# Optimization experiments

Hardware: AMD Instinct MI355X
Metric: run time of the kernel (lower is better)

The kernel has to match this reference:

```python
import jax, jax.numpy as jnp
import numpy as np
from jax import lax

START_TAG = 29
STOP_TAG = 30
PAD_TAG = 31
NEG_INF = -10000.0


def setup_inputs() -> dict:
    key = jax.random.key(0)
    k_feat, k_trans, k_len = jax.random.split(key, 3)
    S, B, T = 1024, 1024, 32
    feats = jax.random.normal(k_feat, (S, B, T), dtype=jnp.float32)
    # left-aligned padding mask with random lengths in [S//2, S]
    lengths = jax.random.randint(k_len, (B,), S // 2, S + 1)
    mask = (jnp.arange(S)[:, None] < lengths[None, :]).astype(jnp.float32)  # [S,B]
    transitions = jax.random.normal(k_trans, (T, T), dtype=jnp.float32)
    # replicate the constraint initialization from __init__
    transitions = transitions.at[START_TAG, :].set(NEG_INF)
    transitions = transitions.at[:, STOP_TAG].set(NEG_INF)
    transitions = transitions.at[:, PAD_TAG].set(NEG_INF)
    transitions = transitions.at[PAD_TAG, :].set(NEG_INF)
    transitions = transitions.at[PAD_TAG, STOP_TAG].set(0.0)
    transitions = transitions.at[PAD_TAG, PAD_TAG].set(0.0)
    # zero emissions at padded steps, as _get_lstm_features does (feats * mask)
    feats = feats * mask[:, :, None]
    return {"feats": feats, "mask": mask, "transitions": transitions}


def reference(feats, mask, transitions):
    """CRF forward algorithm (log partition) + Viterbi max-score scan.

    feats: [S, B, T] emission scores, mask: [S, B] float, transitions: [T, T]
    (transitions[i, j] = score of transitioning from tag j to tag i).
    Returns (logZ [B], best_score [B], pointers [S, B, T] int32).
    """
    S, B, T = feats.shape

    alpha0 = jnp.full((B, T), NEG_INF, dtype=feats.dtype).at[:, START_TAG].set(0.0)

    def fwd_step(alpha, xs):
        feat, m = xs  # feat [B,T], m [B]
        # alpha_t[b, i, j] = alpha[b, j] + transitions[i, j] + feat[b, i]
        alpha_t = alpha[:, None, :] + transitions[None, :, :] + feat[:, :, None]
        new = jax.nn.logsumexp(alpha_t, axis=-1)  # [B,T]
        m = m[:, None]
        return new * m + alpha * (1.0 - m), None

    alpha, _ = lax.scan(fwd_step, alpha0, (feats, mask))
    logZ = jax.nn.logsumexp(alpha + transitions[STOP_TAG][None, :], axis=-1)  # [B]

    def vit_step(scores, xs):
        feat, m = xs
        scores_t = scores[:, None, :] + transitions[None, :, :]  # [B,T,T]
        best = jnp.max(scores_t, axis=-1)                        # [B,T]
        ptr = jnp.argmax(scores_t, axis=-1).astype(jnp.int32)    # [B,T]
        scores_t = best + feat
        m = m[:, None]
        return scores_t * m + scores * (1.0 - m), ptr

    scores0 = jnp.full((B, T), NEG_INF, dtype=feats.dtype).at[:, START_TAG].set(0.0)
    scores, pointers = lax.scan(vit_step, scores0, (feats, mask))
    scores = scores + transitions[STOP_TAG][None, :]
    best_score = jnp.max(scores, axis=-1)  # [B]
    return logZ, best_score, pointers
```

## Files before the change

### kernel.cpp

```cpp
#include <hip/hip_runtime.h>


#define SS 1024
#define BB 1024
#define TT 32
#define POFF (2 * BB)

static __device__ __forceinline__ float fastrcp(float x) {
#if __has_builtin(__builtin_amdgcn_rcpf)
  return __builtin_amdgcn_rcpf(x);
#else
  return 1.0f / x;
#endif
}

__global__ __launch_bounds__(64, 1) void crf3_kernel(
    const float* __restrict__ feats,
    const float* __restrict__ mask,
    const float* __restrict__ trans,
    float* __restrict__ out) {

  const int l  = threadIdx.x;
  const int h  = l >> 5;
  const int i  = l & 31;
  const int b0 = blockIdx.x * 2;
  const int b  = b0 + h;

  __shared__ __align__(16) float row[64];

  const float* fbase = feats + (size_t)b0 * TT + l;
  const float* mbase = mask + b;
  const float t_stop = trans[30 * TT + i];

  float fA[4], mA[4], fB[4], mB[4];
#pragma unroll
  for (int u = 0; u < 4; ++u) {
    fA[u] = fbase[(size_t)u * (BB * TT)];
    mA[u] = mbase[(size_t)u * BB];
    fB[u] = fbase[(size_t)(u + 4) * (BB * TT)];
    mB[u] = mbase[(size_t)(u + 4) * BB];
  }

  if (blockIdx.y == 0) {
    float er[32];
#pragma unroll
    for (int k = 0; k < 32; ++k)
      er[k] = __expf(trans[i * TT + k]);

    float p = (i == 29) ? 1.0f : 0.0f;
    float C = 0.0f;

    auto fstep = [&](float fv, float mv) {
      bool act = (mv != 0.0f);
      float ef = __expf(fv);
      row[l] = p;
      __builtin_amdgcn_wave_barrier();
      const float4* q = (const float4*)&row[h * 32];
      float4 q0 = q[0], q1 = q[1], q2 = q[2], q3 = q[3];
      float4 q4 = q[4], q5 = q[5], q6 = q[6], q7 = q[7];
      __builtin_amdgcn_wave_barrier();
      float q0c = fmaxf(q0.x, 1e-20f);
      float r = fastrcp(q0c);
      float a0 = er[0] * q0.x, a1 = er[1] * q0.y;
      float a2 = er[2] * q0.z, a3 = er[3] * q0.w;
      a0 = fmaf(er[4],  q1.x, a0); a1 = fmaf(er[5],  q1.y, a1);
      a2 = fmaf(er[6],  q1.z, a2); a3 = fmaf(er[7],  q1.w, a3);
      a0 = fmaf(er[8],  q2.x, a0); a1 = fmaf(er[9],  q2.y, a1);
      a2 = fmaf(er[10], q2.z, a2); a3 = fmaf(er[11], q2.w, a3);
      a0 = fmaf(er[12], q3.x, a0); a1 = fmaf(er[13], q3.y, a1);
      a2 = fmaf(er[14], q3.z, a2); a3 = fmaf(er[15], q3.w, a3);
      a0 = fmaf(er[16], q4.x, a0); a1 = fmaf(er[17], q4.y, a1);
      a2 = fmaf(er[18], q4.z, a2); a3 = fmaf(er[19], q4.w, a3);
      a0 = fmaf(er[20], q5.x, a0); a1 = fmaf(er[21], q5.y, a1);
      a2 = fmaf(er[22], q5.z, a2); a3 = fmaf(er[23], q5.w, a3);
      a0 = fmaf(er[24], q6.x, a0); a1 = fmaf(er[25], q6.y, a1);
      a2 = fmaf(er[26], q6.z, a2); a3 = fmaf(er[27], q6.w, a3);
      a0 = fmaf(er[28], q7.x, a0); a1 = fmaf(er[29], q7.y, a1);
      a2 = fmaf(er[30], q7.z, a2); a3 = fmaf(er[31], q7.w, a3);
      float D = (a0 + a1) + (a2 + a3);
      float pn = D * r * ef;
      p = act ? pn : p;
      C += act ? __logf(q0c) : 0.0f;
    };

#pragma unroll 1
    for (int s = 0; s < SS; s += 8) {
      if (__ballot(mA[0] != 0.0f) == 0ull) goto fwd_done;
#pragma unroll
      for (int u = 0; u < 4; ++u) fstep(fA[u], mA[u]);
#pragma unroll
      for (int u = 0; u < 4; ++u) {
        int su = s + 8 + u; su = (su < SS) ? su : 0;
        fA[u] = fbase[(size_t)su * (BB * TT)];
        mA[u] = mbase[(size_t)su * BB];
      }
      if (__ballot(mB[0] != 0.0f) == 0ull) goto fwd_done;
#pragma unroll
      for (int u = 0; u < 4; ++u) fstep(fB[u], mB[u]);
#pragma unroll
      for (int u = 0; u < 4; ++u) {
        int su = s + 12 + u; su = (su < SS) ? su : 0;
        fB[u] = fbase[(size_t)su * (BB * TT)];
        mB[u] = mbase[(size_t)su * BB];
      }
    }
fwd_done:
    {
      float alpha = C + __logf(p);
      float v = alpha + t_stop;
      float M2 = v;
#pragma unroll
      for (int d = 1; d < 32; d <<= 1) M2 = fmaxf(M2, __shfl_xor(M2, d, 64));
      float e = __expf(v - M2);
#pragma unroll
      for (int d = 1; d < 32; d <<= 1) e += __shfl_xor(e, d, 64);
      if (i == 0) out[b] = M2 + __logf(e);
    }
    return;
  }

  {
    float tr[32];
#pragma unroll
    for (int k = 0; k < 32; ++k) tr[k] = trans[i * TT + k];

    float sc = (i == 29) ? 0.0f : -10000.0f;
    int s_exit = SS;

    auto vstep = [&](float& best, int& ptr) {
      row[l] = sc;
      __builtin_amdgcn_wave_barrier();
      const float4* q = (const float4*)&row[h * 32];
      float4 q0 = q[0], q1 = q[1], q2 = q[2], q3 = q[3];
      float4 q4 = q[4], q5 = q[5], q6 = q[6], q7 = q[7];
      __builtin_amdgcn_wave_barrier();
      float v[32];
      v[0]  = q0.x + tr[0];  v[1]  = q0.y + tr[1];
      v[2]  = q0.z + tr[2];  v[3]  = q0.w + tr[3];
      v[4]  = q1.x + tr[4];  v[5]  = q1.y + tr[5];
      v[6]  = q1.z + tr[6];  v[7]  = q1.w + tr[7];
      v[8]  = q2.x + tr[8];  v[9]  = q2.y + tr[9];
      v[10] = q2.z + tr[10]; v[11] = q2.w + tr[11];
      v[12] = q3.x + tr[12]; v[13] = q3.y + tr[13];
      v[14] = q3.z + tr[14]; v[15] = q3.w + tr[15];
      v[16] = q4.x + tr[16]; v[17] = q4.y + tr[17];
      v[18] = q4.z + tr[18]; v[19] = q4.w + tr[19];
      v[20] = q5.x + tr[20]; v[21] = q5.y + tr[21];
      v[22] = q5.z + tr[22]; v[23] = q5.w + tr[23];
      v[24] = q6.x + tr[24]; v[25] = q6.y + tr[25];
      v[26] = q6.z + tr[26]; v[27] = q6.w + tr[27];
      v[28] = q7.x + tr[28]; v[29] = q7.y + tr[29];
      v[30] = q7.z + tr[30]; v[31] = q7.w + tr[31];
      int ix[32];
#pragma unroll
      for (int k = 0; k < 32; ++k) ix[k] = k;
#pragma unroll
      for (int st = 1; st < 32; st <<= 1) {
#pragma unroll
        for (int k = 0; k < 32; k += 2 * st) {
          bool t = v[k + st] > v[k];
          v[k]  = t ? v[k + st] : v[k];
          ix[k] = t ? ix[k + st] : ix[k];
        }
      }
      best = v[0];
      ptr  = ix[0];
    };

#pragma unroll 1
    for (int s = 0; s < SS; s += 8) {
      if (__ballot(mA[0] != 0.0f) == 0ull) { s_exit = s; goto vtail; }
#pragma unroll
      for (int u = 0; u < 4; ++u) {
        float best; int ptr;
        vstep(best, ptr);
        out[POFF + (size_t)(s + u) * (BB * TT) + b0 * TT + l] = (float)ptr;
        sc = (mA[u] != 0.0f) ? (best + fA[u]) : sc;
      }
#pragma unroll
      for (int u = 0; u < 4; ++u) {
        int su = s + 8 + u; su = (su < SS) ? su : 0;
        fA[u] = fbase[(size_t)su * (BB * TT)];
        mA[u] = mbase[(size_t)su * BB];
      }
      if (__ballot(mB[0] != 0.0f) == 0ull) { s_exit = s + 4; goto vtail; }
#pragma unroll
      for (int u = 0; u < 4; ++u) {
        float best; int ptr;
        vstep(best, ptr);
        out[POFF + (size_t)(s + 4 + u) * (BB * TT) + b0 * TT + l] = (float)ptr;
        sc = (mB[u] != 0.0f) ? (best + fB[u]) : sc;
      }
#pragma unroll
      for (int u = 0; u < 4; ++u) {
        int su = s + 12 + u; su = (su < SS) ? su : 0;
        fB[u] = fbase[(size_t)su * (BB * TT)];
        mB[u] = mbase[(size_t)su * BB];
      }
    }
vtail:
    {
      float tb; int tp;
      vstep(tb, tp);
      float tj = (float)tp;
      for (int s2 = s_exit; s2 < SS; ++s2)
        out[POFF + (size_t)s2 * (BB * TT) + b0 * TT + l] = tj;

      float w = sc + t_stop;
#pragma unroll
      for (int d = 1; d < 32; d <<= 1) w = fmaxf(w, __shfl_xor(w, d, 64));
      if (i == 0) out[BB + b] = w;
    }
  }
}

extern "C" void kernel_launch(void* const* d_in, const int* in_sizes, int n_in,
                              void* d_out, int out_size, void* d_ws, size_t ws_size,
                              hipStream_t stream) {
  const float* feats = (const float*)d_in[0];
  const float* msk   = (const float*)d_in[1];
  const float* trans = (const float*)d_in[2];
  float* out = (float*)d_out;
  (void)in_sizes; (void)n_in; (void)out_size; (void)d_ws; (void)ws_size;
  crf3_kernel<<<dim3(BB / 2, 2), dim3(64), 0, stream>>>(feats, msk, trans, out);
}
```

Measured before the change: 544.2 us.

## Replace LDS row broadcast with DPP/bpermute cross-lane gathers and remapped lanes

Tags are remapped across lanes so that each batch row's 32 tags span two 16-lane rows in different wave halves. Each step's all-to-all broadcast of the state vector now uses DPP permutations within a 16-lane row plus ds_bpermute across halves, replacing the LDS store/load round trip. The transition tables are stored pre-permuted to match the gathered order. The Viterbi argmax becomes a max tree followed by a min-index tree, and the forward normalizer comes from a bpermute of the previous step's state. The gather needs 16 bpermutes per step, which may cost as much as the LDS traffic it removes.

```diff
diff --git a/kernel.cpp b/kernel.cpp
--- a/kernel.cpp
+++ b/kernel.cpp
@@ -14,21 +14,58 @@
 #endif
 }
 
-__global__ __launch_bounds__(64, 1) void crf3_kernel(
+#define DPP_QX1   0xB1
+#define DPP_QX2   0x4E
+#define DPP_QX3   0x1B
+#define DPP_RMIR  0x140
+#define DPP_RHMIR 0x141
+
+template <int CTRL>
+static __device__ __forceinline__ float dppx(float x) {
+  return __int_as_float(
+      __builtin_amdgcn_update_dpp(0, __float_as_int(x), CTRL, 0xF, 0xF, false));
+}
+
+static __device__ __forceinline__ float bperm(int byteaddr, float x) {
+  return __int_as_float(
+      __builtin_amdgcn_ds_bpermute(byteaddr, __float_as_int(x)));
+}
+
+static __device__ __forceinline__ void gather16(float x, float r[16]) {
+  r[0]  = x;
+  r[1]  = dppx<DPP_QX1>(x);
+  r[2]  = dppx<DPP_QX2>(x);
+  r[3]  = dppx<DPP_QX3>(x);
+  r[7]  = dppx<DPP_RHMIR>(x);
+  r[6]  = dppx<DPP_QX1>(r[7]);
+  r[5]  = dppx<DPP_QX2>(r[7]);
+  r[4]  = dppx<DPP_QX3>(r[7]);
+  r[15] = dppx<DPP_RMIR>(x);
+  r[14] = dppx<DPP_QX1>(r[15]);
+  r[13] = dppx<DPP_QX2>(r[15]);
+  r[12] = dppx<DPP_QX3>(r[15]);
+  r[8]  = dppx<DPP_RHMIR>(r[15]);
+  r[9]  = dppx<DPP_QX1>(r[8]);
+  r[10] = dppx<DPP_QX2>(r[8]);
+  r[11] = dppx<DPP_QX3>(r[8]);
+}
+
+__global__ __launch_bounds__(64, 1) void crf4_kernel(
     const float* __restrict__ feats,
     const float* __restrict__ mask,
     const float* __restrict__ trans,
     float* __restrict__ out) {
 
   const int l  = threadIdx.x;
-  const int h  = l >> 5;
-  const int i  = l & 31;
+  const int t0 = l & 15;
+  const int i  = t0 | ((l >> 1) & 16);
+  const int h  = (l >> 4) & 1;
   const int b0 = blockIdx.x * 2;
   const int b  = b0 + h;
-
-  __shared__ __align__(16) float row[64];
-
-  const float* fbase = feats + (size_t)b0 * TT + l;
+  const int bp32 = (l ^ 32) << 2;
+  const bool hiHalf = (l & 32) != 0;
+
+  const float* fbase = feats + (size_t)b * TT + i;
   const float* mbase = mask + b;
   const float t_stop = trans[30 * TT + i];
 
@@ -42,45 +79,51 @@
   }
 
   if (blockIdx.y == 0) {
-    float er[32];
-#pragma unroll
-    for (int k = 0; k < 32; ++k)
-      er[k] = __expf(trans[i * TT + k]);
-
-    float p = (i == 29) ? 1.0f : 0.0f;
-    float C = 0.0f;
+    float eOwn[16], eOth[16];
+#pragma unroll
+    for (int m = 0; m < 16; ++m) {
+      int x = t0 ^ m;
+      int jown = hiHalf ? (16 | x) : x;
+      int joth = hiHalf ? x : (16 | x);
+      eOwn[m] = __expf(trans[i * TT + jown]);
+      eOth[m] = __expf(trans[i * TT + joth]);
+    }
+
+    float p   = (i == 29) ? 1.0f : 0.0f;
+    float C   = 0.0f;
+    float q0f = 0.0f;
 
     auto fstep = [&](float fv, float mv) {
       bool act = (mv != 0.0f);
       float ef = __expf(fv);
-      row[l] = p;
-      __builtin_amdgcn_wave_barrier();
-      const float4* q = (const float4*)&row[h * 32];
-      float4 q0 = q[0], q1 = q[1], q2 = q[2], q3 = q[3];
-      float4 q4 = q[4], q5 = q[5], q6 = q[6], q7 = q[7];
-      __builtin_amdgcn_wave_barrier();
-      float q0c = fmaxf(q0.x, 1e-20f);
-      float r = fastrcp(q0c);
-      float a0 = er[0] * q0.x, a1 = er[1] * q0.y;
-      float a2 = er[2] * q0.z, a3 = er[3] * q0.w;
-      a0 = fmaf(er[4],  q1.x, a0); a1 = fmaf(er[5],  q1.y, a1);
-      a2 = fmaf(er[6],  q1.z, a2); a3 = fmaf(er[7],  q1.w, a3);
-      a0 = fmaf(er[8],  q2.x, a0); a1 = fmaf(er[9],  q2.y, a1);
-      a2 = fmaf(er[10], q2.z, a2); a3 = fmaf(er[11], q2.w, a3);
-      a0 = fmaf(er[12], q3.x, a0); a1 = fmaf(er[13], q3.y, a1);
-      a2 = fmaf(er[14], q3.z, a2); a3 = fmaf(er[15], q3.w, a3);
-      a0 = fmaf(er[16], q4.x, a0); a1 = fmaf(er[17], q4.y, a1);
-      a2 = fmaf(er[18], q4.z, a2); a3 = fmaf(er[19], q4.w, a3);
-      a0 = fmaf(er[20], q5.x, a0); a1 = fmaf(er[21], q5.y, a1);
-      a2 = fmaf(er[22], q5.z, a2); a3 = fmaf(er[23], q5.w, a3);
-      a0 = fmaf(er[24], q6.x, a0); a1 = fmaf(er[25], q6.y, a1);
-      a2 = fmaf(er[26], q6.z, a2); a3 = fmaf(er[27], q6.w, a3);
-      a0 = fmaf(er[28], q7.x, a0); a1 = fmaf(er[29], q7.y, a1);
-      a2 = fmaf(er[30], q7.z, a2); a3 = fmaf(er[31], q7.w, a3);
-      float D = (a0 + a1) + (a2 + a3);
-      float pn = D * r * ef;
+      float r16[16];
+      gather16(p, r16);
+      float oth[16];
+#pragma unroll
+      for (int m = 0; m < 16; ++m) oth[m] = bperm(bp32, r16[m]);
+      float a0 = eOwn[0] * r16[0], a1 = eOwn[1] * r16[1];
+      float a2 = eOwn[2] * r16[2], a3 = eOwn[3] * r16[3];
+#pragma unroll
+      for (int m = 4; m < 16; m += 4) {
+        a0 = fmaf(eOwn[m + 0], r16[m + 0], a0);
+        a1 = fmaf(eOwn[m + 1], r16[m + 1], a1);
+        a2 = fmaf(eOwn[m + 2], r16[m + 2], a2);
+        a3 = fmaf(eOwn[m + 3], r16[m + 3], a3);
+      }
+#pragma unroll
+      for (int m = 0; m < 16; m += 4) {
+        a0 = fmaf(eOth[m + 0], oth[m + 0], a0);
+        a1 = fmaf(eOth[m + 1], oth[m + 1], a1);
+        a2 = fmaf(eOth[m + 2], oth[m + 2], a2);
+        a3 = fmaf(eOth[m + 3], oth[m + 3], a3);
+      }
+      float D   = (a0 + a1) + (a2 + a3);
+      float q0c = fmaxf(q0f, 1e-20f);
+      float r   = fastrcp(q0c);
+      float pn  = D * r * ef;
       p = act ? pn : p;
       C += act ? __logf(q0c) : 0.0f;
+      q0f = bperm((l & 16) << 2, p);
     };
 
 #pragma unroll 1
@@ -109,93 +152,108 @@
       float alpha = C + __logf(p);
       float v = alpha + t_stop;
       float M2 = v;
-#pragma unroll
-      for (int d = 1; d < 32; d <<= 1) M2 = fmaxf(M2, __shfl_xor(M2, d, 64));
+      M2 = fmaxf(M2, __shfl_xor(M2, 1, 64));
+      M2 = fmaxf(M2, __shfl_xor(M2, 2, 64));
+      M2 = fmaxf(M2, __shfl_xor(M2, 4, 64));
+      M2 = fmaxf(M2, __shfl_xor(M2, 8, 64));
+      M2 = fmaxf(M2, __shfl_xor(M2, 32, 64));
       float e = __expf(v - M2);
-#pragma unroll
-      for (int d = 1; d < 32; d <<= 1) e += __shfl_xor(e, d, 64);
+      e += __shfl_xor(e, 1, 64);
+      e += __shfl_xor(e, 2, 64);
+      e += __shfl_xor(e, 4, 64);
+      e += __shfl_xor(e, 8, 64);
+      e += __shfl_xor(e, 32, 64);
       if (i == 0) out[b] = M2 + __logf(e);
     }
     return;
   }
 
   {
-    float tr[32];
-#pragma unroll
-    for (int k = 0; k < 32; ++k) tr[k] = trans[i * TT + k];
+    float tOwn[16], tOth[16];
+    int   gOwn[16], gOth[16];
+#pragma unroll
+    for (int m = 0; m < 16; ++m) {
+      int x = t0 ^ m;
+      int jown = hiHalf ? (16 | x) : x;
+      int joth = hiHalf ? x : (16 | x);
+      tOwn[m] = trans[i * TT + jown];
+      tOth[m] = trans[i * TT + joth];
+      gOwn[m] = jown;
+      gOth[m] = joth;
+    }
 
     float sc = (i == 29) ? 0.0f : -10000.0f;
     int s_exit = SS;
+    float* outp = out + POFF + (size_t)b * TT + i;
 
     auto vstep = [&](float& best, int& ptr) {
-      row[l] = sc;
-      __builtin_amdgcn_wave_barrier();
-      const float4* q = (const float4*)&row[h * 32];
-      float4 q0 = q[0], q1 = q[1], q2 = q[2], q3 = q[3];
-      float4 q4 = q[4], q5 = q[5], q6 = q[6], q7 = q[7];
-      __builtin_amdgcn_wave_barrier();
-      float v[32];
-      v[0]  = q0.x + tr[0];  v[1]  = q0.y + tr[1];
-      v[2]  = q0.z + tr[2];  v[3]  = q0.w + tr[3];
-      v[4]  = q1.x + tr[4];  v[5]  = q1.y + tr[5];
-      v[6]  = q1.z + tr[6];  v[7]  = q1.w + tr[7];
-      v[8]  = q2.x + tr[8];  v[9]  = q2.y + tr[9];
-      v[10] = q2.z + tr[10]; v[11] = q2.w + tr[11];
-      v[12] = q3.x + tr[12]; v[13] = q3.y + tr[13];
-      v[14] = q3.z + tr[14]; v[15] = q3.w + tr[15];
-      v[16] = q4.x + tr[16]; v[17] = q4.y + tr[17];
-      v[18] = q4.z + tr[18]; v[19] = q4.w + tr[19];
-      v[20] = q5.x + tr[20]; v[21] = q5.y + tr[21];
-      v[22] = q5.z + tr[22]; v[23] = q5.w + tr[23];
-      v[24] = q6.x + tr[24]; v[25] = q6.y + tr[25];
-      v[26] = q6.z + tr[26]; v[27] = q6.w + tr[27];
-      v[28] = q7.x + tr[28]; v[29] = q7.y + tr[29];
-      v[30] = q7.z + tr[30]; v[31] = q7.w + tr[31];
+      float r16[16];
+      gather16(sc, r16);
+      float vv[32];
+#pragma unroll
+      for (int m = 0; m < 16; ++m) vv[16 + m] = bperm(bp32, r16[m]) + tOth[m];
+#pragma unroll
+      for (int m = 0; m < 16; ++m) vv[m] = r16[m] + tOwn[m];
+      float w0[8], w1[8];
+#pragma unroll
+      for (int k = 0; k < 8; ++k) w0[k] = fmaxf(vv[k], vv[k + 8]);
+#pragma unroll
+      for (int st = 4; st >= 1; st >>= 1)
+#pragma unroll
+        for (int k = 0; k < st; ++k) w0[k] = fmaxf(w0[k], w0[k + st]);
+#pragma unroll
+      for (int k = 0; k < 8; ++k) w1[k] = fmaxf(vv[16 + k], vv[24 + k]);
+#pragma unroll
+      for (int st = 4; st >= 1; st >>= 1)
+#pragma unroll
+        for (int k = 0; k < st; ++k) w1[k] = fmaxf(w1[k], w1[k + st]);
+      float mx = fmaxf(w0[0], w1[0]);
       int ix[32];
 #pragma unroll
-      for (int k = 0; k < 32; ++k) ix[k] = k;
-#pragma unroll
-      for (int st = 1; st < 32; st <<= 1) {
-#pragma unroll
-        for (int k = 0; k < 32; k += 2 * st) {
-          bool t = v[k + st] > v[k];
-          v[k]  = t ? v[k + st] : v[k];
-          ix[k] = t ? ix[k + st] : ix[k];
-        }
-      }
-      best = v[0];
-      ptr  = ix[0];
+      for (int m = 0; m < 16; ++m) {
+        ix[m]      = (vv[m]      == mx) ? gOwn[m] : 63;
+        ix[16 + m] = (vv[16 + m] == mx) ? gOth[m] : 63;
+      }
+      int u[16];
+#pragma unroll
+      for (int k = 0; k < 16; ++k) u[k] = (ix[k] < ix[k + 16]) ? ix[k] : ix[k + 16];
+#pragma unroll
+      for (int st = 8; st >= 1; st >>= 1)
+#pragma unroll
+        for (int k = 0; k < st; ++k) u[k] = (u[k] < u[k + st]) ? u[k] : u[k + st];
+      best = mx;
+      ptr  = u[0];
     };
 
 #pragma unroll 1
     for (int s = 0; s < SS; s += 8) {
       if (__ballot(mA[0] != 0.0f) == 0ull) { s_exit = s; goto vtail; }
 #pragma unroll
-      for (int u = 0; u < 4; ++u) {
+      for (int u2 = 0; u2 < 4; ++u2) {
         float best; int ptr;
         vstep(best, ptr);
-        out[POFF + (size_t)(s + u) * (BB * TT) + b0 * TT + l] = (float)ptr;
-        sc = (mA[u] != 0.0f) ? (best + fA[u]) : sc;
-      }
-#pragma unroll
-      for (int u = 0; u < 4; ++u) {
-        int su = s + 8 + u; su = (su < SS) ? su : 0;
-        fA[u] = fbase[(size_t)su * (BB * TT)];
-        mA[u] = mbase[(size_t)su * BB];
+        outp[(size_t)(s + u2) * (BB * TT)] = (float)ptr;
+        sc = (mA[u2] != 0.0f) ? (best + fA[u2]) : sc;
+      }
+#pragma unroll
+      for (int u2 = 0; u2 < 4; ++u2) {
+        int su = s + 8 + u2; su = (su < SS) ? su : 0;
+        fA[u2] = fbase[(size_t)su * (BB * TT)];
+        mA[u2] = mbase[(size_t)su * BB];
       }
       if (__ballot(mB[0] != 0.0f) == 0ull) { s_exit = s + 4; goto vtail; }
 #pragma unroll
-      for (int u = 0; u < 4; ++u) {
+      for (int u2 = 0; u2 < 4; ++u2) {
         float best; int ptr;
         vstep(best, ptr);
-        out[POFF + (size_t)(s + 4 + u) * (BB * TT) + b0 * TT + l] = (float)ptr;
-        sc = (mB[u] != 0.0f) ? (best + fB[u]) : sc;
-      }
-#pragma unroll
-      for (int u = 0; u < 4; ++u) {
-        int su = s + 12 + u; su = (su < SS) ? su : 0;
-        fB[u] = fbase[(size_t)su * (BB * TT)];
-        mB[u] = mbase[(size_t)su * BB];
+        outp[(size_t)(s + 4 + u2) * (BB * TT)] = (float)ptr;
+        sc = (mB[u2] != 0.0f) ? (best + fB[u2]) : sc;
+      }
+#pragma unroll
+      for (int u2 = 0; u2 < 4; ++u2) {
+        int su = s + 12 + u2; su = (su < SS) ? su : 0;
+        fB[u2] = fbase[(size_t)su * (BB * TT)];
+        mB[u2] = mbase[(size_t)su * BB];
       }
     }
 vtail:
@@ -204,11 +262,14 @@
       vstep(tb, tp);
       float tj = (float)tp;
       for (int s2 = s_exit; s2 < SS; ++s2)
-        out[POFF + (size_t)s2 * (BB * TT) + b0 * TT + l] = tj;
+        outp[(size_t)s2 * (BB * TT)] = tj;
 
       float w = sc + t_stop;
-#pragma unroll
-      for (int d = 1; d < 32; d <<= 1) w = fmaxf(w, __shfl_xor(w, d, 64));
+      w = fmaxf(w, __shfl_xor(w, 1, 64));
+      w = fmaxf(w, __shfl_xor(w, 2, 64));
+      w = fmaxf(w, __shfl_xor(w, 4, 64));
+      w = fmaxf(w, __shfl_xor(w, 8, 64));
+      w = fmaxf(w, __shfl_xor(w, 32, 64));
       if (i == 0) out[BB + b] = w;
     }
   }
@@ -222,5 +283,5 @@
   const float* trans = (const float*)d_in[2];
   float* out = (float*)d_out;
   (void)in_sizes; (void)n_in; (void)out_size; (void)d_ws; (void)ws_size;
-  crf3_kernel<<<dim3(BB / 2, 2), dim3(64), 0, stream>>>(feats, msk, trans, out);
-}
+  crf4_kernel<<<dim3(BB / 2, 2), dim3(64), 0, stream>>>(feats, msk, trans, out);
+}
```

Measured after the change: 695.3 us. 1.28x slower.
